# Optimization experiments

Measured on AMD Instinct MI355X. Metric: run time of the kernel, lower is better.

The kernel has to match this reference:

```python
import jax, jax.numpy as jnp
import numpy as np

N_NODES = 100000
N_EDGES = 1700000


def _build_csr(rng, n, e):
    row = rng.integers(0, n, size=e).astype(np.int64)
    col = rng.integers(0, n, size=e).astype(np.int32)
    order = np.argsort(row, kind='stable')
    row = row[order]
    col = col[order]
    rowptr = np.searchsorted(row, np.arange(n + 1)).astype(np.int32)
    return rowptr, col


def setup_inputs() -> dict:
    key = jax.random.key(0)
    k1, k2, k3, k4 = jax.random.split(key, 4)
    rng = np.random.default_rng(0)
    rowptr, colind = _build_csr(rng, N_NODES, N_EDGES)
    F_in, H, C = 256, 128, 16
    return {
        'x': jax.random.normal(k1, (N_NODES, F_in), dtype=jnp.float32),
        'edge_weight': jax.random.uniform(k2, (N_EDGES,), dtype=jnp.float32) + 0.5,
        'W1': jax.random.normal(k3, (F_in, H), dtype=jnp.float32) * (1.0 / np.sqrt(F_in)),
        'b1': jnp.zeros((H,), dtype=jnp.float32),
        'W2': jax.random.normal(k4, (H, C), dtype=jnp.float32) * (1.0 / np.sqrt(H)),
        'b2': jnp.zeros((C,), dtype=jnp.float32),
        'rowptr': jnp.asarray(rowptr),
        'colind': jnp.asarray(colind),
    }


def _rowids_from_rowptr(rowptr, n_edges):
    # CSR rowptr -> per-nnz row index, jit-friendly
    return (jnp.searchsorted(rowptr, jnp.arange(n_edges, dtype=rowptr.dtype), side='right') - 1).astype(jnp.int32)


def reference(x, edge_weight, W1, b1, W2, b2, rowptr, colind):
    n = x.shape[0]
    e = colind.shape[0]
    row = _rowids_from_rowptr(rowptr, e)
    col = colind

    # GCN symmetric normalization: D^-1/2 A D^-1/2 (cached=True -> shared by both layers)
    deg = jax.ops.segment_sum(edge_weight, row, num_segments=n)
    dinv = jnp.where(deg > 0, jax.lax.rsqrt(deg), 0.0)
    w = dinv[row] * edge_weight * dinv[col]

    def gcn_layer(h, W, b):
        h = h @ W                                   # [n, d_out]
        # SpMM: out[r] = sum_e w[e] * h[col[e]]
        msg = w[:, None] * h[col]                   # [e, d_out] gather
        return jax.ops.segment_sum(msg, row, num_segments=n) + b

    h = jax.nn.relu(gcn_layer(x, W1, b1))
    # dropout is identity in eval mode
    out = gcn_layer(h, W2, b2)
    return jax.nn.log_softmax(out, axis=1)
```

## Files before the change

### kernel.cpp

```cpp
#include <hip/hip_runtime.h>
#include <hip/hip_bf16.h>

#define F_IN 256
#define HDIM 128
#define CDIM 16

typedef unsigned short u16;
typedef unsigned int u32;

typedef __attribute__((ext_vector_type(8))) short bf16x8;
typedef __attribute__((ext_vector_type(4))) float f32x4;

__device__ __forceinline__ float bf2f(u32 v) {
    u32 u = v << 16;
    float f;
    __builtin_memcpy(&f, &u, 4);
    return f;
}
__device__ __forceinline__ u16 f2bf(float f) {
    u32 u;
    __builtin_memcpy(&u, &f, 4);
    u32 r = (u + 0x7FFFu + ((u >> 16) & 1u)) >> 16;
    return (u16)r;
}
__device__ __forceinline__ u32 cvtpk(float lo, float hi) {
    u32 r;
    asm("v_cvt_pk_bf16_f32 %0, %1, %2" : "=v"(r) : "v"(lo), "v"(hi));
    return r;
}

__global__ __launch_bounds__(256) void k_dinv(const float* __restrict__ ew,
                                              const int* __restrict__ rowptr,
                                              float* __restrict__ dinv, int n) {
    int sg = threadIdx.x >> 4;
    int sl = threadIdx.x & 15;
    int r = blockIdx.x * 16 + sg;
    if (r >= n) return;
    int s = rowptr[r], e = rowptr[r + 1];
    float acc = 0.f;
    for (int i = s + sl; i < e; i += 16) acc += ew[i];
    acc += __shfl_xor(acc, 1);
    acc += __shfl_xor(acc, 2);
    acc += __shfl_xor(acc, 4);
    acc += __shfl_xor(acc, 8);
    if (sl == 0) dinv[r] = (acc > 0.f) ? rsqrtf(acc) : 0.f;
}

__global__ __launch_bounds__(256) void k_w(const float* __restrict__ ew,
                                           const int* __restrict__ rowptr,
                                           const int* __restrict__ col,
                                           const float* __restrict__ dinv,
                                           float* __restrict__ wn, int n) {
    int sg = threadIdx.x >> 4;
    int sl = threadIdx.x & 15;
    int r = blockIdx.x * 16 + sg;
    if (r >= n) return;
    float dr = dinv[r];
    int s = rowptr[r], e = rowptr[r + 1];
    for (int i = s + sl; i < e; i += 16)
        wn[i] = dr * ew[i] * dinv[col[i]];
}

__global__ void k_prepw1(const float* __restrict__ W1, u16* __restrict__ W1T) {
    int idx = blockIdx.x * blockDim.x + threadIdx.x;
    if (idx >= HDIM * F_IN) return;
    int f = idx >> 8;
    int k = idx & 255;
    W1T[idx] = f2bf(W1[(size_t)k * HDIM + f]);
}

__global__ __launch_bounds__(512, 4) void k_gemm1(const float* __restrict__ x,
                                                  const u16* __restrict__ W1T,
                                                  u16* __restrict__ T1, int n) {
    __shared__ u16 Bs[HDIM * F_IN];

    int tid = threadIdx.x;
#pragma unroll
    for (int it = 0; it < 8; it++) {
        int o16 = it * 512 + tid;
        u32 o = (u32)o16 * 16;
        u32 swz = o ^ (((o >> 9) & 7u) << 4);
        uint4 v = ((const uint4*)W1T)[o16];
        *(uint4*)((char*)Bs + swz) = v;
    }
    __syncthreads();

    int wave = tid >> 6;
    int lane = tid & 63;
    int lr = lane & 15;
    int kg = lane >> 4;
    int r0 = blockIdx.x * 256 + wave * 32;
    if (r0 >= n) return;

    f32x4 acc[2][8];
#pragma unroll
    for (int rg = 0; rg < 2; rg++)
#pragma unroll
        for (int ct = 0; ct < 8; ct++) acc[rg][ct] = (f32x4){0.f, 0.f, 0.f, 0.f};

    int rowc[2];
#pragma unroll
    for (int rg = 0; rg < 2; rg++) {
        int row = r0 + rg * 16 + lr;
        rowc[rg] = row < n ? row : (n - 1);
    }

#pragma unroll
    for (int kk = 0; kk < F_IN / 32; kk++) {
        bf16x8 afrag[2];
#pragma unroll
        for (int rg = 0; rg < 2; rg++) {
            const float4* ap = (const float4*)(x + (size_t)rowc[rg] * F_IN + kg * 8 + kk * 32);
            float4 alo = ap[0];
            float4 ahi = ap[1];
            u32 q0 = cvtpk(alo.x, alo.y);
            u32 q1 = cvtpk(alo.z, alo.w);
            u32 q2 = cvtpk(ahi.x, ahi.y);
            u32 q3 = cvtpk(ahi.z, ahi.w);
            u32 qa[4] = {q0, q1, q2, q3};
            __builtin_memcpy(&afrag[rg], qa, 16);
        }
#pragma unroll
        for (int ct = 0; ct < 8; ct++) {
            u32 a = (u32)(ct * 16 + lr) * (F_IN * 2) + (u32)kg * 16 + (u32)kk * 64;
            u32 aswz = a ^ (((a >> 9) & 7u) << 4);
            bf16x8 bfrag = *(const bf16x8*)((const char*)Bs + aswz);
#pragma unroll
            for (int rg = 0; rg < 2; rg++)
                acc[rg][ct] = __builtin_amdgcn_mfma_f32_16x16x32_bf16(afrag[rg], bfrag, acc[rg][ct], 0, 0, 0);
        }
    }

#pragma unroll
    for (int rg = 0; rg < 2; rg++) {
        int rbase = r0 + rg * 16 + kg * 4;
#pragma unroll
        for (int ct = 0; ct < 8; ct++) {
#pragma unroll
            for (int i = 0; i < 4; i += 2) {
                u32 q = cvtpk(acc[rg][ct][i], acc[rg][ct][i + 1]);
                int row0 = rbase + i;
                int row1 = rbase + i + 1;
                if (row0 < n) T1[(size_t)row0 * HDIM + ct * 16 + lr] = (u16)(q & 0xFFFFu);
                if (row1 < n) T1[(size_t)row1 * HDIM + ct * 16 + lr] = (u16)(q >> 16);
            }
        }
    }
}

__global__ __launch_bounds__(256) void k_spmm1(const u16* __restrict__ T1,
                                               const float* __restrict__ wn,
                                               const int* __restrict__ rowptr,
                                               const int* __restrict__ col,
                                               const float* __restrict__ b1,
                                               u16* __restrict__ H, int n) {
    int wave = threadIdx.x >> 6;
    int lane = threadIdx.x & 63;
    int r = blockIdx.x * 4 + wave;
    if (r >= n) return;
    int es = lane >> 4;
    int fl = lane & 15;

    int s = rowptr[r], e = rowptr[r + 1];
    int deg = e - s;
    int nwin = deg >> 4;
    float a[8];
#pragma unroll
    for (int j = 0; j < 8; j++) a[j] = 0.f;

#define ACCUM(w_, p_) do { \
        a[0] += (w_) * bf2f((p_).x & 0xFFFFu); a[1] += (w_) * bf2f((p_).x >> 16); \
        a[2] += (w_) * bf2f((p_).y & 0xFFFFu); a[3] += (w_) * bf2f((p_).y >> 16); \
        a[4] += (w_) * bf2f((p_).z & 0xFFFFu); a[5] += (w_) * bf2f((p_).z >> 16); \
        a[6] += (w_) * bf2f((p_).w & 0xFFFFu); a[7] += (w_) * bf2f((p_).w >> 16); \
    } while (0)

    int i = s + es;
    for (int w = 0; w < nwin; w++, i += 16) {
        float w0 = wn[i];      int c0 = col[i];
        float w1 = wn[i + 4];  int c1 = col[i + 4];
        float w2 = wn[i + 8];  int c2 = col[i + 8];
        float w3 = wn[i + 12]; int c3 = col[i + 12];
        uint4 p0 = *(const uint4*)(T1 + (size_t)c0 * HDIM + fl * 8);
        uint4 p1 = *(const uint4*)(T1 + (size_t)c1 * HDIM + fl * 8);
        uint4 p2 = *(const uint4*)(T1 + (size_t)c2 * HDIM + fl * 8);
        uint4 p3 = *(const uint4*)(T1 + (size_t)c3 * HDIM + fl * 8);
        ACCUM(w0, p0);
        ACCUM(w1, p1);
        ACCUM(w2, p2);
        ACCUM(w3, p3);
    }
    if (deg & 15) {
        int i1 = i + 4, i2 = i + 8, i3 = i + 12;
        int j0 = i  < e ? i  : (e - 1);
        int j1 = i1 < e ? i1 : (e - 1);
        int j2 = i2 < e ? i2 : (e - 1);
        int j3 = i3 < e ? i3 : (e - 1);
        float w0 = i  < e ? wn[j0] : 0.f;
        float w1 = i1 < e ? wn[j1] : 0.f;
        float w2 = i2 < e ? wn[j2] : 0.f;
        float w3 = i3 < e ? wn[j3] : 0.f;
        int c0 = col[j0], c1 = col[j1], c2 = col[j2], c3 = col[j3];
        uint4 p0 = *(const uint4*)(T1 + (size_t)c0 * HDIM + fl * 8);
        uint4 p1 = *(const uint4*)(T1 + (size_t)c1 * HDIM + fl * 8);
        uint4 p2 = *(const uint4*)(T1 + (size_t)c2 * HDIM + fl * 8);
        uint4 p3 = *(const uint4*)(T1 + (size_t)c3 * HDIM + fl * 8);
        ACCUM(w0, p0);
        ACCUM(w1, p1);
        ACCUM(w2, p2);
        ACCUM(w3, p3);
    }
#undef ACCUM

#pragma unroll
    for (int j = 0; j < 8; j++) {
        a[j] += __shfl_xor(a[j], 16);
        a[j] += __shfl_xor(a[j], 32);
    }

    if (es == 0) {
        const float4* bb = (const float4*)(b1 + fl * 8);
        float4 blo = bb[0], bhi = bb[1];
        float v0 = a[0] + blo.x, v1 = a[1] + blo.y;
        float v2 = a[2] + blo.z, v3 = a[3] + blo.w;
        float v4 = a[4] + bhi.x, v5 = a[5] + bhi.y;
        float v6 = a[6] + bhi.z, v7 = a[7] + bhi.w;
        v0 = v0 > 0.f ? v0 : 0.f; v1 = v1 > 0.f ? v1 : 0.f;
        v2 = v2 > 0.f ? v2 : 0.f; v3 = v3 > 0.f ? v3 : 0.f;
        v4 = v4 > 0.f ? v4 : 0.f; v5 = v5 > 0.f ? v5 : 0.f;
        v6 = v6 > 0.f ? v6 : 0.f; v7 = v7 > 0.f ? v7 : 0.f;
        uint4 o;
        o.x = cvtpk(v0, v1); o.y = cvtpk(v2, v3);
        o.z = cvtpk(v4, v5); o.w = cvtpk(v6, v7);
        *(uint4*)(H + (size_t)r * HDIM + fl * 8) = o;
    }
}

__global__ __launch_bounds__(256) void k_gemm2(const u16* __restrict__ H,
                                               const float* __restrict__ W2,
                                               float* __restrict__ U, int n) {
    int rl = threadIdx.x >> 4;
    int f = threadIdx.x & 15;
    int row = blockIdx.x * 16 + rl;
    if (row >= n) return;
    const u32* hr = (const u32*)(H + (size_t)row * HDIM);
    float acc = 0.f;
    for (int k2 = 0; k2 < HDIM / 2; k2++) {
        u32 pr = hr[k2];
        float h0 = bf2f(pr & 0xFFFFu);
        float h1 = bf2f(pr >> 16);
        acc += h0 * W2[(size_t)(k2 * 2) * CDIM + f];
        acc += h1 * W2[(size_t)(k2 * 2 + 1) * CDIM + f];
    }
    U[(size_t)row * CDIM + f] = acc;
}

__global__ __launch_bounds__(256) void k_out(const float* __restrict__ U,
                                             const float* __restrict__ wn,
                                             const int* __restrict__ rowptr,
                                             const int* __restrict__ col,
                                             const float* __restrict__ b2,
                                             float* __restrict__ out, int n) {
    int wave = threadIdx.x >> 6;
    int lane = threadIdx.x & 63;
    int r = blockIdx.x * 4 + wave;
    if (r >= n) return;
    int es = lane >> 3;
    int fl = lane & 7;
    int s = rowptr[r], e = rowptr[r + 1];
    int deg = e - s;
    int nwin = deg >> 4;
    float a0 = 0.f, a1 = 0.f;

    int i = s + es;
    for (int w = 0; w < nwin; w++, i += 16) {
        float w0 = wn[i];     int c0 = col[i];
        float w1 = wn[i + 8]; int c1 = col[i + 8];
        float2 u0 = *(const float2*)(U + (size_t)c0 * CDIM + fl * 2);
        float2 u1 = *(const float2*)(U + (size_t)c1 * CDIM + fl * 2);
        a0 += w0 * u0.x; a1 += w0 * u0.y;
        a0 += w1 * u1.x; a1 += w1 * u1.y;
    }
    if (deg & 15) {
        int i1 = i + 8;
        int j0 = i  < e ? i  : (e - 1);
        int j1 = i1 < e ? i1 : (e - 1);
        float w0 = i  < e ? wn[j0] : 0.f;
        float w1 = i1 < e ? wn[j1] : 0.f;
        int c0 = col[j0], c1 = col[j1];
        float2 u0 = *(const float2*)(U + (size_t)c0 * CDIM + fl * 2);
        float2 u1 = *(const float2*)(U + (size_t)c1 * CDIM + fl * 2);
        a0 += w0 * u0.x; a1 += w0 * u0.y;
        a0 += w1 * u1.x; a1 += w1 * u1.y;
    }

    a0 += __shfl_xor(a0, 8);  a1 += __shfl_xor(a1, 8);
    a0 += __shfl_xor(a0, 16); a1 += __shfl_xor(a1, 16);
    a0 += __shfl_xor(a0, 32); a1 += __shfl_xor(a1, 32);

    float2 bp = ((const float2*)b2)[fl];
    float v0 = a0 + bp.x;
    float v1 = a1 + bp.y;

    float m = fmaxf(v0, v1);
    m = fmaxf(m, __shfl_xor(m, 1));
    m = fmaxf(m, __shfl_xor(m, 2));
    m = fmaxf(m, __shfl_xor(m, 4));
    float ss = __expf(v0 - m) + __expf(v1 - m);
    ss += __shfl_xor(ss, 1);
    ss += __shfl_xor(ss, 2);
    ss += __shfl_xor(ss, 4);
    float ls = __logf(ss);
    if (es == 0) {
        float2 res = {v0 - m - ls, v1 - m - ls};
        *(float2*)(out + (size_t)r * CDIM + fl * 2) = res;
    }
}

extern "C" void kernel_launch(void* const* d_in, const int* in_sizes, int n_in,
                              void* d_out, int out_size, void* d_ws, size_t ws_size,
                              hipStream_t stream) {
    const float* x      = (const float*)d_in[0];
    const float* ew     = (const float*)d_in[1];
    const float* W1     = (const float*)d_in[2];
    const float* b1     = (const float*)d_in[3];
    const float* W2     = (const float*)d_in[4];
    const float* b2     = (const float*)d_in[5];
    const int*   rowptr = (const int*)d_in[6];
    const int*   colind = (const int*)d_in[7];

    int n = in_sizes[6] - 1;
    int E = in_sizes[7];

    auto align256 = [](size_t v) { return (v + 255) & ~(size_t)255; };
    char* p = (char*)d_ws;
    float* dinv = (float*)p; p += align256((size_t)n * 4);
    float* wn   = (float*)p; p += align256((size_t)E * 4);
    u16*   T1   = (u16*)p;   p += align256((size_t)n * HDIM * 2);
    u16*   H    = (u16*)p;   p += align256((size_t)n * HDIM * 2);
    float* U    = (float*)p; p += align256((size_t)n * CDIM * 4);
    u16*   W1T  = (u16*)p;   p += align256((size_t)HDIM * F_IN * 2);
    float* out  = (float*)d_out;

    k_dinv<<<(n + 15) / 16, 256, 0, stream>>>(ew, rowptr, dinv, n);
    k_w<<<(n + 15) / 16, 256, 0, stream>>>(ew, rowptr, colind, dinv, wn, n);
    k_prepw1<<<(HDIM * F_IN + 255) / 256, 256, 0, stream>>>(W1, W1T);

    k_gemm1<<<(n + 255) / 256, 512, 0, stream>>>(x, W1T, T1, n);

    k_spmm1<<<(n + 3) / 4, 256, 0, stream>>>(T1, wn, rowptr, colind, b1, H, n);
    k_gemm2<<<(n + 15) / 16, 256, 0, stream>>>(H, W2, U, n);
    k_out<<<(n + 3) / 4, 256, 0, stream>>>(U, wn, rowptr, colind, b2, out, n);
}
```

Before: 181.0 us.

## Stage x tiles into LDS via global_load_lds in gemm1 with smaller blocks

The first GEMM now streams each 32-wide K slice of x into a swizzled LDS buffer using direct global-to-LDS loads, then reads A fragments from LDS. Before, each lane loaded its fragments from global memory itself. Blocks shrink from 512 threads and 256 rows to 256 threads and 128 rows, with a new occupancy hint. The aim is coalesced loads of x. The cost is two barriers per K step, a full vmcnt wait with no double buffering, and the 64KB W1 copy being reloaded by twice as many blocks.

```diff
diff --git a/kernel.cpp b/kernel.cpp
--- a/kernel.cpp
+++ b/kernel.cpp
@@ -69,28 +69,28 @@
     W1T[idx] = f2bf(W1[(size_t)k * HDIM + f]);
 }
 
-__global__ __launch_bounds__(512, 4) void k_gemm1(const float* __restrict__ x,
+__global__ __launch_bounds__(256, 2) void k_gemm1(const float* __restrict__ x,
                                                   const u16* __restrict__ W1T,
                                                   u16* __restrict__ T1, int n) {
     __shared__ u16 Bs[HDIM * F_IN];
+    __shared__ float Xs[128 * 32];
 
     int tid = threadIdx.x;
 #pragma unroll
-    for (int it = 0; it < 8; it++) {
-        int o16 = it * 512 + tid;
+    for (int it = 0; it < 16; it++) {
+        int o16 = it * 256 + tid;
         u32 o = (u32)o16 * 16;
         u32 swz = o ^ (((o >> 9) & 7u) << 4);
         uint4 v = ((const uint4*)W1T)[o16];
         *(uint4*)((char*)Bs + swz) = v;
     }
-    __syncthreads();
 
     int wave = tid >> 6;
     int lane = tid & 63;
     int lr = lane & 15;
     int kg = lane >> 4;
-    int r0 = blockIdx.x * 256 + wave * 32;
-    if (r0 >= n) return;
+    int r0 = blockIdx.x * 128;
+    int wr0 = r0 + wave * 32;
 
     f32x4 acc[2][8];
 #pragma unroll
@@ -98,28 +98,42 @@
 #pragma unroll
         for (int ct = 0; ct < 8; ct++) acc[rg][ct] = (f32x4){0.f, 0.f, 0.f, 0.f};
 
-    int rowc[2];
-#pragma unroll
-    for (int rg = 0; rg < 2; rg++) {
-        int row = r0 + rg * 16 + lr;
-        rowc[rg] = row < n ? row : (n - 1);
-    }
-
-#pragma unroll
-    for (int kk = 0; kk < F_IN / 32; kk++) {
+    int srow[4], sslot[4];
+#pragma unroll
+    for (int it = 0; it < 4; it++) {
+        int row = (wave << 5) + (it << 3) + (lane >> 3);
+        int grow = r0 + row;
+        srow[it] = grow < n ? grow : (n - 1);
+        sslot[it] = (lane & 7) ^ (row & 7);
+    }
+
+    for (int kk = 0; kk < 8; kk++) {
+#pragma unroll
+        for (int it = 0; it < 4; it++) {
+            const float* src = x + (size_t)srow[it] * F_IN + kk * 32 + sslot[it] * 4;
+            void* ldst = (void*)((char*)Xs + (wave << 12) + (it << 10));
+            __builtin_amdgcn_global_load_lds(src, ldst, 16, 0, 0);
+        }
+        asm volatile("s_waitcnt vmcnt(0)");
+        __syncthreads();
+
         bf16x8 afrag[2];
 #pragma unroll
         for (int rg = 0; rg < 2; rg++) {
-            const float4* ap = (const float4*)(x + (size_t)rowc[rg] * F_IN + kg * 8 + kk * 32);
-            float4 alo = ap[0];
-            float4 ahi = ap[1];
-            u32 q0 = cvtpk(alo.x, alo.y);
-            u32 q1 = cvtpk(alo.z, alo.w);
-            u32 q2 = cvtpk(ahi.x, ahi.y);
-            u32 q3 = cvtpk(ahi.z, ahi.w);
+            int row = wave * 32 + rg * 16 + lr;
+            u32 a = (u32)row * 128 + (u32)kg * 32;
+            u32 x0 = a ^ (((u32)row & 7u) << 4);
+            u32 x1 = (a + 16) ^ (((u32)row & 7u) << 4);
+            float4 lo = *(const float4*)((const char*)Xs + x0);
+            float4 hi = *(const float4*)((const char*)Xs + x1);
+            u32 q0 = cvtpk(lo.x, lo.y);
+            u32 q1 = cvtpk(lo.z, lo.w);
+            u32 q2 = cvtpk(hi.x, hi.y);
+            u32 q3 = cvtpk(hi.z, hi.w);
             u32 qa[4] = {q0, q1, q2, q3};
             __builtin_memcpy(&afrag[rg], qa, 16);
         }
+
 #pragma unroll
         for (int ct = 0; ct < 8; ct++) {
             u32 a = (u32)(ct * 16 + lr) * (F_IN * 2) + (u32)kg * 16 + (u32)kk * 64;
@@ -129,11 +143,12 @@
             for (int rg = 0; rg < 2; rg++)
                 acc[rg][ct] = __builtin_amdgcn_mfma_f32_16x16x32_bf16(afrag[rg], bfrag, acc[rg][ct], 0, 0, 0);
         }
+        __syncthreads();
     }
 
 #pragma unroll
     for (int rg = 0; rg < 2; rg++) {
-        int rbase = r0 + rg * 16 + kg * 4;
+        int rbase = wr0 + rg * 16 + kg * 4;
 #pragma unroll
         for (int ct = 0; ct < 8; ct++) {
 #pragma unroll
@@ -346,7 +361,7 @@
     k_w<<<(n + 15) / 16, 256, 0, stream>>>(ew, rowptr, colind, dinv, wn, n);
     k_prepw1<<<(HDIM * F_IN + 255) / 256, 256, 0, stream>>>(W1, W1T);
 
-    k_gemm1<<<(n + 255) / 256, 512, 0, stream>>>(x, W1T, T1, n);
+    k_gemm1<<<(n + 127) / 128, 256, 0, stream>>>(x, W1T, T1, n);
 
     k_spmm1<<<(n + 3) / 4, 256, 0, stream>>>(T1, wn, rowptr, colind, b1, H, n);
     k_gemm2<<<(n + 15) / 16, 256, 0, stream>>>(H, W2, U, n);
```

Result: no change. 181.6 us (+0.3%).
